# Optimization experiments

Measured on AMD Instinct MI355X. Metric: run time of the kernel, lower is better.

Reference implementation:

```python
import jax, jax.numpy as jnp
import numpy as np

DG = 8   # deformable groups
KK = 9   # 3x3 kernel positions


def conv3x3(x, w, b):
    # x: [B,C,H,W], w: [O,I,3,3] -> SAME conv, stride 1
    y = jax.lax.conv_general_dilated(x, w, (1, 1), 'SAME',
                                     dimension_numbers=('NCHW', 'OIHW', 'NCHW'))
    return y + b[None, :, None, None]


def modulated_deform_conv(x, offset, mask, w, b):
    # x: [B,C,H,W]; offset: [B,DG,KK,2,H,W] (dy,dx per group/kernel-pos);
    # mask: [B,DG,KK,H,W]; w: [O,C,3,3]; groups=1, stride=1, pad=1, dil=1.
    B, C, H, W = x.shape
    cg = C // DG  # channels per deformable group
    dy = offset[:, :, :, 0]  # [B,DG,KK,H,W]
    dx = offset[:, :, :, 1]
    ky, kx = jnp.meshgrid(jnp.arange(3), jnp.arange(3), indexing='ij')
    ky = (ky.reshape(KK) - 1).astype(x.dtype)  # kernel y offsets (pad=1)
    kx = (kx.reshape(KK) - 1).astype(x.dtype)
    py = dy + jnp.arange(H, dtype=x.dtype).reshape(1, 1, 1, H, 1) + ky.reshape(1, 1, KK, 1, 1)
    px = dx + jnp.arange(W, dtype=x.dtype).reshape(1, 1, 1, 1, W) + kx.reshape(1, 1, KK, 1, 1)
    y0 = jnp.floor(py)
    x0 = jnp.floor(px)
    ly = py - y0  # bilinear fractions
    lx = px - x0
    y0i = y0.astype(jnp.int32)
    x0i = x0.astype(jnp.int32)
    xf = x.reshape(B, DG, cg, H * W)

    def gather(yi, xi):
        # zero padding outside the image (per-corner validity)
        valid = ((yi >= 0) & (yi < H) & (xi >= 0) & (xi < W)).astype(x.dtype)
        idx = jnp.clip(yi, 0, H - 1) * W + jnp.clip(xi, 0, W - 1)  # [B,DG,KK,H,W]
        g = jnp.take_along_axis(xf, idx.reshape(B, DG, 1, KK * H * W), axis=-1)
        return g.reshape(B, DG, cg, KK, H, W) * valid[:, :, None]

    v = (((1 - ly) * (1 - lx))[:, :, None] * gather(y0i, x0i)
         + ((1 - ly) * lx)[:, :, None] * gather(y0i, x0i + 1)
         + (ly * (1 - lx))[:, :, None] * gather(y0i + 1, x0i)
         + (ly * lx)[:, :, None] * gather(y0i + 1, x0i + 1))
    v = (v * mask[:, :, None]).reshape(B, C, KK, H, W)  # modulated im2col
    out = jnp.einsum('bckhw,ock->bohw', v, w.reshape(w.shape[0], C, KK))
    return out + b[None, :, None, None]


def setup_inputs() -> dict:
    key = jax.random.key(0)
    ks = jax.random.split(key, 6)
    B, C, H, W = 8, 64, 128, 128
    f = lambda k, s: jax.random.normal(k, s, dtype=jnp.float32)
    return {
        'cat_fea': f(ks[0], (B, C, H, W)),
        'f_fea': f(ks[1], (B, C, H, W)),
        'w_off2d': f(ks[2], (C, C, 3, 3)) * 0.05,
        'b_off2d': jnp.zeros((C,), jnp.float32),
        'w_coff': f(ks[3], (3 * DG * KK, C, 3, 3)) * 0.01,  # small => near-zero offsets, as in DCNv2Pack init
        'b_coff': jnp.zeros((3 * DG * KK,), jnp.float32),
        'w_dconv': f(ks[4], (C, C, 3, 3)) * 0.05,
        'b_dconv': jnp.zeros((C,), jnp.float32),
    }


def reference(cat_fea, f_fea, w_off2d, b_off2d, w_coff, b_coff, w_dconv, b_dconv):
    # offset1 = self.off2d_1(cat_fea)
    offset_feat = conv3x3(cat_fea, w_off2d, b_off2d)
    # DCNv2Pack: conv_offset on the extra feature, chunk into o1,o2,mask
    off = conv3x3(offset_feat, w_coff, b_coff)  # [B, 3*DG*KK, H, W]
    o1, o2, m = jnp.split(off, 3, axis=1)
    B, _, H, W = off.shape
    # offset = cat(o1,o2); CUDA kernel reads channel ((g*KK+i)*2 + {0:y,1:x})
    offset = jnp.concatenate([o1, o2], axis=1).reshape(B, DG, KK, 2, H, W)
    mask = jax.nn.sigmoid(m).reshape(B, DG, KK, H, W)
    return modulated_deform_conv(f_fea, offset, mask, w_dconv, b_dconv)
```

## Files before the change

### kernel.cpp

```cpp
#include <hip/hip_runtime.h>
#include <math.h>

typedef __attribute__((ext_vector_type(4))) float f32x4;
typedef __attribute__((ext_vector_type(8))) short bf16x8;
typedef __attribute__((ext_vector_type(2))) _Float16 f16x2;
typedef __attribute__((ext_vector_type(8))) _Float16 f16x8;

#define HH 128
#define WW 128
#define HWSZ 16384
#define BHW 131072
#define BB 8

__device__ __forceinline__ float bf2f(ushort u) {
    union { uint i; float f; } x; x.i = ((uint)u) << 16; return x.f;
}
__device__ __forceinline__ ushort f2bf(float f) {
    union { float f; uint i; } x; x.f = f;
    uint r = (x.i + 0x7fffu + ((x.i >> 16) & 1u)) >> 16;
    return (ushort)r;
}
__device__ __forceinline__ ushort f2h_bits(float f) {
    union { _Float16 h; ushort u; } x; x.h = (_Float16)f; return x.u;
}

template<int F16>
__global__ __launch_bounds__(256) void to_gp_k(const float* __restrict__ x,
                                               ushort* __restrict__ y) {
    __shared__ ushort lds[64][66];
    int blk = blockIdx.x;
    int b = blk >> 8;
    int hw0 = (blk & 255) << 6;
    int t = threadIdx.x;
    int lane = t & 63;
    int q = t >> 6;
#pragma unroll
    for (int i = 0; i < 16; i++) {
        int c = i * 4 + q;
        float v = x[((size_t)(b * 64 + c) << 14) + hw0 + lane];
        lds[c][lane] = F16 ? f2h_bits(v) : f2bf(v);
    }
    __syncthreads();
#pragma unroll
    for (int it = 0; it < 2; it++) {
        int id = it * 256 + t;
        int cg = id >> 6;
        int px = id & 63;
        uint pk[4];
#pragma unroll
        for (int j = 0; j < 4; j++)
            pk[j] = (uint)lds[cg * 8 + 2 * j][px] | ((uint)lds[cg * 8 + 2 * j + 1][px] << 16);
        *(uint4*)(y + ((((size_t)b * 8 + cg) << 14) + hw0 + px) * 8) = *(uint4*)pk;
    }
}

template<int F16>
__global__ __launch_bounds__(256) void prep_wa(const float* __restrict__ w,
                                               ushort* __restrict__ wa, int Co, int Co_pad) {
    int idx = blockIdx.x * 256 + threadIdx.x;
    if (idx >= Co_pad * 576) return;
    int co = idx / 576, r = idx % 576;
    int kk = r >> 6, ci = r & 63;
    ushort v = 0;
    if (co < Co) {
        float f = w[(co * 64 + ci) * 9 + kk];
        v = F16 ? f2h_bits(f) : f2bf(f);
    }
    wa[idx] = v;
}

template<int COT, int MODE>
__global__ __launch_bounds__(256, 4) void conv_gemm3_k(
    const ushort* __restrict__ xt, const ushort* __restrict__ wa,
    const float* __restrict__ bias, ushort* __restrict__ y,
    uint* __restrict__ dyxp, ushort* __restrict__ mpl, int Cout) {
    constexpr int WCO = COT / 4;
    constexpr int NN = WCO / 16;
    constexpr int NA = COT / 32;
    __shared__ ushort Al[COT * 64];
    __shared__ ushort Bt[128 * 64];
    int t = threadIdx.x;
    int orig = blockIdx.x;
    int blk = (orig & 7) * 128 + (orig >> 3);
    int b = blk >> 7;
    int h = blk & 127;
    int cot = blockIdx.y;
    int lane = t & 63;
    int wv = t >> 6;
    int lg = lane >> 4;
    int lr = lane & 15;
    int rs = (lr & 7) << 4;
    int asw = ((lane & 7) ^ (lane >> 3)) << 4;
    const char* wab = (const char*)wa;

    f32x4 acc[NN][8];
#pragma unroll
    for (int n = 0; n < NN; n++)
#pragma unroll
        for (int j = 0; j < 8; j++) acc[n][j] = f32x4{0, 0, 0, 0};

#pragma unroll 1
    for (int kk = 0; kk < 9; kk++) {
        int ky = kk / 3;
        int kx = kk - ky * 3;
        __syncthreads();
#pragma unroll
        for (int a = 0; a < NA; a++) {
            int rb = wv * WCO + a * 8;
            const char* g = wab + (size_t)(cot * COT + rb + (lane >> 3)) * 1152 + kk * 128 + asw;
            __builtin_amdgcn_global_load_lds(
                (const __attribute__((address_space(1))) void*)g,
                (__attribute__((address_space(3))) void*)((char*)Al + rb * 128),
                16, 0, 0);
        }
        int hy = h + ky - 1;
        bool vr = (unsigned)hy < 128u;
#pragma unroll
        for (int i = 0; i < 4; i++) {
            int id = i * 256 + t;
            int px = id & 127;
            int cg = id >> 7;
            int wx = px + kx - 1;
            uint4 v = {0u, 0u, 0u, 0u};
            if (vr && (unsigned)wx < 128u)
                v = *(const uint4*)(xt + ((((size_t)b * 8 + cg) << 14) + (hy << 7) + wx) * 8);
            *(uint4*)((char*)Bt + px * 128 + ((cg * 16) ^ ((px & 7) << 4))) = v;
        }
        __syncthreads();
        bf16x8 a0[NN], a1[NN];
#pragma unroll
        for (int n = 0; n < NN; n++) {
            int ar = wv * WCO + n * 16 + lr;
            a0[n] = *(const bf16x8*)((char*)Al + ar * 128 + ((lg * 16) ^ rs));
            a1[n] = *(const bf16x8*)((char*)Al + ar * 128 + ((lg * 16 + 64) ^ rs));
        }
#pragma unroll
        for (int j = 0; j < 8; j++) {
            int pr = j * 16 + lr;
            bf16x8 b0 = *(const bf16x8*)((char*)Bt + pr * 128 + ((lg * 16) ^ rs));
            bf16x8 b1 = *(const bf16x8*)((char*)Bt + pr * 128 + ((lg * 16 + 64) ^ rs));
#pragma unroll
            for (int n = 0; n < NN; n++) {
                acc[n][j] = __builtin_amdgcn_mfma_f32_16x16x32_bf16(a0[n], b0, acc[n][j], 0, 0, 0);
                acc[n][j] = __builtin_amdgcn_mfma_f32_16x16x32_bf16(a1[n], b1, acc[n][j], 0, 0, 0);
            }
        }
    }

#pragma unroll
    for (int n = 0; n < NN; n++) {
        int co_g = cot * COT + wv * WCO + n * 16 + lg * 4;
        if (co_g < Cout) {
            float bs[4];
#pragma unroll
            for (int r = 0; r < 4; r++) bs[r] = bias[co_g + r];
#pragma unroll
            for (int j = 0; j < 8; j++) {
                int pxl = j * 16 + lr;
                int hw = (h << 7) + pxl;
                int bhw = (b << 14) + hw;
                if (MODE == 0) {
                    int cg = co_g >> 3, cs = co_g & 7;
                    uint2 s2;
                    s2.x = (uint)f2bf(acc[n][j][0] + bs[0]) | ((uint)f2bf(acc[n][j][1] + bs[1]) << 16);
                    s2.y = (uint)f2bf(acc[n][j][2] + bs[2]) | ((uint)f2bf(acc[n][j][3] + bs[3]) << 16);
                    *(uint2*)(y + ((((size_t)b * 8 + cg) << 14) + hw) * 8 + cs) = s2;
                } else if (co_g < 144) {
                    int p0 = co_g >> 1;
                    uint u0 = (uint)f2bf(acc[n][j][0] + bs[0]) | ((uint)f2bf(acc[n][j][1] + bs[1]) << 16);
                    uint u1 = (uint)f2bf(acc[n][j][2] + bs[2]) | ((uint)f2bf(acc[n][j][3] + bs[3]) << 16);
                    dyxp[(size_t)p0 * BHW + bhw] = u0;
                    dyxp[(size_t)(p0 + 1) * BHW + bhw] = u1;
                } else {
#pragma unroll
                    for (int r = 0; r < 4; r++) {
                        float f = 1.f / (1.f + __expf(-(acc[n][j][r] + bs[r])));
                        mpl[(size_t)(co_g - 144 + r) * BHW + bhw] = f2bf(f);
                    }
                }
            }
        }
    }
}

__global__ __launch_bounds__(256) void sample_k(
    const ushort* __restrict__ xg, const uint* __restrict__ dyxp,
    const ushort* __restrict__ mpl, ushort* __restrict__ vt) {
    int p = blockIdx.y;
    int dg = p / 9, tap = p - dg * 9;
    int ky = tap / 3, kx = tap - ky * 3;
    int bx = blockIdx.x;
    int bxs = (bx & 7) * 64 + (bx >> 3);
    int bhw = (bxs << 8) + threadIdx.x;
    int b = bhw >> 14;
    int h = (bhw >> 7) & 127;
    int w = bhw & 127;

    uint dyx = dyxp[(size_t)p * BHW + bhw];
    float m = bf2f(mpl[(size_t)p * BHW + bhw]);
    float dy = bf2f((ushort)(dyx & 0xffff));
    float dx = bf2f((ushort)(dyx >> 16));
    float py = dy + (float)(h + ky - 1);
    float px_ = dx + (float)(w + kx - 1);
    float fy = floorf(py), fx = floorf(px_);
    int y0 = (int)fy, x0 = (int)fx;
    int y1 = y0 + 1, x1 = x0 + 1;
    float ly = py - fy, lx = px_ - fx;
    bool vy0 = (unsigned)y0 < 128u, vy1 = (unsigned)y1 < 128u;
    bool vx0 = (unsigned)x0 < 128u, vx1 = (unsigned)x1 < 128u;
    float w00 = (vy0 && vx0) ? (1.f - ly) * (1.f - lx) * m : 0.f;
    float w01 = (vy0 && vx1) ? (1.f - ly) * lx * m : 0.f;
    float w10 = (vy1 && vx0) ? ly * (1.f - lx) * m : 0.f;
    float w11 = (vy1 && vx1) ? ly * lx * m : 0.f;
    int y0c = min(max(y0, 0), 127), y1c = min(max(y1, 0), 127);
    int x0c = min(max(x0, 0), 127), x1c = min(max(x1, 0), 127);
    const ushort* gb = xg + (((size_t)b * 8 + dg) << 17);
    uint4 q00 = *(const uint4*)(gb + ((y0c << 7) + x0c) * 8);
    uint4 q01 = *(const uint4*)(gb + ((y0c << 7) + x1c) * 8);
    uint4 q10 = *(const uint4*)(gb + ((y1c << 7) + x0c) * 8);
    uint4 q11 = *(const uint4*)(gb + ((y1c << 7) + x1c) * 8);
    const ushort* u00 = (const ushort*)&q00;
    const ushort* u01 = (const ushort*)&q01;
    const ushort* u10 = (const ushort*)&q10;
    const ushort* u11 = (const ushort*)&q11;
    uint pk[4];
#pragma unroll
    for (int c2 = 0; c2 < 4; c2++) {
        float v0 = w00 * bf2f(u00[2*c2])   + w01 * bf2f(u01[2*c2])
                 + w10 * bf2f(u10[2*c2])   + w11 * bf2f(u11[2*c2]);
        float v1 = w00 * bf2f(u00[2*c2+1]) + w01 * bf2f(u01[2*c2+1])
                 + w10 * bf2f(u10[2*c2+1]) + w11 * bf2f(u11[2*c2+1]);
        pk[c2] = (uint)f2bf(v0) | ((uint)f2bf(v1) << 16);
    }
    *(uint4*)(vt + ((size_t)p * BHW + bhw) * 8) = *(uint4*)pk;
}

__global__ __launch_bounds__(256, 3) void dgemm_k(
    const ushort* __restrict__ vt, const ushort* __restrict__ wa,
    const float* __restrict__ bias, float* __restrict__ out) {
    __shared__ ushort Al[64 * 64];
    __shared__ ushort Bt[64 * 64];
    int t = threadIdx.x;
    int orig = blockIdx.x;
    int blk = (orig & 7) * 256 + (orig >> 3);
    int b = blk >> 8;
    int h = (blk >> 1) & 127;
    int w0 = (blk & 1) << 6;
    int lane = t & 63;
    int wv = t >> 6;
    int lg = lane >> 4;
    int lr = lane & 15;
    int rs = (lr & 7) << 4;
    int asw = ((lane & 7) ^ (lane >> 3)) << 4;
    const char* wab = (const char*)wa;
    int bhw0 = (b << 14) + (h << 7) + w0;

    f32x4 acc[4] = {f32x4{0,0,0,0}, f32x4{0,0,0,0}, f32x4{0,0,0,0}, f32x4{0,0,0,0}};

#pragma unroll 1
    for (int kk = 0; kk < 9; kk++) {
        __syncthreads();
#pragma unroll
        for (int a = 0; a < 2; a++) {
            int rb = wv * 16 + a * 8;
            const char* g = wab + (size_t)(rb + (lane >> 3)) * 1152 + kk * 128 + asw;
            __builtin_amdgcn_global_load_lds(
                (const __attribute__((address_space(1))) void*)g,
                (__attribute__((address_space(3))) void*)((char*)Al + rb * 128),
                16, 0, 0);
        }
        uint4 v0 = *(const uint4*)(vt + ((size_t)(wv * 9 + kk) * BHW + bhw0 + lane) * 8);
        uint4 v1 = *(const uint4*)(vt + ((size_t)((wv + 4) * 9 + kk) * BHW + bhw0 + lane) * 8);
        int swl = (lane & 7) << 4;
        *(uint4*)((char*)Bt + lane * 128 + ((wv * 16) ^ swl)) = v0;
        *(uint4*)((char*)Bt + lane * 128 + (((wv + 4) * 16) ^ swl)) = v1;
        __syncthreads();
        int ar = wv * 16 + lr;
        bf16x8 a0 = *(const bf16x8*)((char*)Al + ar * 128 + ((lg * 16) ^ rs));
        bf16x8 a1 = *(const bf16x8*)((char*)Al + ar * 128 + ((lg * 16 + 64) ^ rs));
#pragma unroll
        for (int j = 0; j < 4; j++) {
            int pr = j * 16 + lr;
            bf16x8 b0 = *(const bf16x8*)((char*)Bt + pr * 128 + ((lg * 16) ^ rs));
            bf16x8 b1 = *(const bf16x8*)((char*)Bt + pr * 128 + ((lg * 16 + 64) ^ rs));
            acc[j] = __builtin_amdgcn_mfma_f32_16x16x32_bf16(a0, b0, acc[j], 0, 0, 0);
            acc[j] = __builtin_amdgcn_mfma_f32_16x16x32_bf16(a1, b1, acc[j], 0, 0, 0);
        }
    }

    int co_g = wv * 16 + lg * 4;
    float bs[4];
#pragma unroll
    for (int r = 0; r < 4; r++) bs[r] = bias[co_g + r];
#pragma unroll
    for (int j = 0; j < 4; j++) {
        int hw = (h << 7) + w0 + j * 16 + lr;
#pragma unroll
        for (int r = 0; r < 4; r++) {
            out[((size_t)(b * 64 + co_g + r) << 14) + hw] = acc[j][r] + bs[r];
        }
    }
}

__global__ __launch_bounds__(256, 3) void deform_reg3_k(
    const ushort* __restrict__ xg, const uint* __restrict__ dyxp,
    const ushort* __restrict__ mpl, const ushort* __restrict__ wa,
    const float* __restrict__ bias, float* __restrict__ out) {
    int t = threadIdx.x;
    int orig = blockIdx.x;
    int blk = (orig & 7) * 256 + (orig >> 3);
    int b = blk >> 8;
    int h = (blk >> 1) & 127;
    int w0 = (blk & 1) << 6;
    int lane = t & 63;
    int wv = t >> 6;
    int lg = lane >> 4;
    int lr = lane & 15;
    int wabs = w0 + wv * 16 + lr;
    int bhw = (b << 14) + (h << 7) + wabs;

    uint dyxv[18];
    float mv[18];
#pragma unroll
    for (int c = 0; c < 18; c++) {
        int dg = ((c & 1) << 2) + lg;
        int tap = c >> 1;
        dyxv[c] = dyxp[(size_t)(dg * 9 + tap) * BHW + bhw];
        mv[c] = bf2f(mpl[(size_t)(dg * 9 + tap) * BHW + bhw]);
    }

    uint4 qg[2][4];
    f32x4 wt4[2];
    f16x8 afr[2][4];
    f32x4 acc[4] = {f32x4{0,0,0,0}, f32x4{0,0,0,0}, f32x4{0,0,0,0}, f32x4{0,0,0,0}};

#define DPRE(c) do {                                                            \
    const int tap = (c) >> 1;                                                   \
    const int ky = tap / 3;                                                     \
    const int kx = tap - ky * 3;                                                \
    int dg = (((c) & 1) << 2) + lg;                                             \
    uint dyx = dyxv[(c)];                                                       \
    float dy = bf2f((ushort)(dyx & 0xffff));                                    \
    float dx = bf2f((ushort)(dyx >> 16));                                       \
    float py = dy + (float)(h + ky - 1);                                        \
    float px_ = dx + (float)(wabs + kx - 1);                                    \
    float fy = floorf(py), fx = floorf(px_);                                    \
    int y0 = (int)fy, x0 = (int)fx;                                             \
    int y1 = y0 + 1, x1 = x0 + 1;                                               \
    int y0c = min(max(y0, 0), 127), y1c = min(max(y1, 0), 127);                 \
    int x0c = min(max(x0, 0), 127), x1c = min(max(x1, 0), 127);                 \
    const ushort* gb = xg + (((size_t)b * 8 + dg) << 17);                       \
    qg[(c) & 1][0] = *(const uint4*)(gb + ((y0c << 7) + x0c) * 8);              \
    qg[(c) & 1][1] = *(const uint4*)(gb + ((y0c << 7) + x1c) * 8);              \
    qg[(c) & 1][2] = *(const uint4*)(gb + ((y1c << 7) + x0c) * 8);              \
    qg[(c) & 1][3] = *(const uint4*)(gb + ((y1c << 7) + x1c) * 8);              \
    float ly = py - fy, lx = px_ - fx;                                          \
    bool vy0 = (unsigned)y0 < 128u, vy1 = (unsigned)y1 < 128u;                  \
    bool vx0 = (unsigned)x0 < 128u, vx1 = (unsigned)x1 < 128u;                  \
    float m = mv[(c)];                                                          \
    f32x4 wv4;                                                                  \
    wv4[0] = (vy0 && vx0) ? (1.f - ly) * (1.f - lx) * m : 0.f;                  \
    wv4[1] = (vy0 && vx1) ? (1.f - ly) * lx * m : 0.f;                          \
    wv4[2] = (vy1 && vx0) ? ly * (1.f - lx) * m : 0.f;                          \
    wv4[3] = (vy1 && vx1) ? ly * lx * m : 0.f;                                  \
    wt4[(c) & 1] = wv4;                                                         \
} while (0)

#define APRE(c) do {                                                            \
    const ushort* wac = wa + (c) * 32 + lg * 8;                                 \
    _Pragma("unroll")                                                           \
    for (int n = 0; n < 4; n++)                                                 \
        afr[(c) & 1][n] = *(const f16x8*)(wac + (size_t)(n * 16 + lr) * 576);   \
} while (0)

    DPRE(0);
    APRE(0);

#pragma unroll
    for (int c = 0; c < 18; c++) {
        if (c < 17) {
            DPRE(c + 1);
            APRE(c + 1);
        }
        __builtin_amdgcn_sched_barrier(0);
        f32x4 wc = wt4[c & 1];
        _Float16 wh0 = (_Float16)wc[0], wh1 = (_Float16)wc[1];
        _Float16 wh2 = (_Float16)wc[2], wh3 = (_Float16)wc[3];
        f16x2 w0p = {wh0, wh0}, w1p = {wh1, wh1}, w2p = {wh2, wh2}, w3p = {wh3, wh3};
        union { uint4 u4; uint u[4]; } c00, c01, c10, c11;
        c00.u4 = qg[c & 1][0]; c01.u4 = qg[c & 1][1];
        c10.u4 = qg[c & 1][2]; c11.u4 = qg[c & 1][3];
        union { f16x2 p[4]; f16x8 v; } bf;
#pragma unroll
        for (int c2 = 0; c2 < 4; c2++) {
            union { uint u; f16x2 h; } h00, h01, h10, h11;
            h00.u = c00.u[c2]; h01.u = c01.u[c2];
            h10.u = c10.u[c2]; h11.u = c11.u[c2];
            bf.p[c2] = h00.h * w0p + h01.h * w1p + h10.h * w2p + h11.h * w3p;
        }
#pragma unroll
        for (int n = 0; n < 4; n++)
            acc[n] = __builtin_amdgcn_mfma_f32_16x16x32_f16(afr[c & 1][n], bf.v, acc[n], 0, 0, 0);
    }
#undef DPRE
#undef APRE

    int hw = (h << 7) + wabs;
#pragma unroll
    for (int n = 0; n < 4; n++) {
        int co_g = n * 16 + lg * 4;
#pragma unroll
        for (int r = 0; r < 4; r++) {
            out[((size_t)(b * 64 + co_g + r) << 14) + hw] = acc[n][r] + bias[co_g + r];
        }
    }
}

extern "C" void kernel_launch(void* const* d_in, const int* in_sizes, int n_in,
                              void* d_out, int out_size, void* d_ws, size_t ws_size,
                              hipStream_t stream) {
    const float* cat_fea = (const float*)d_in[0];
    const float* f_fea   = (const float*)d_in[1];
    const float* w_off2d = (const float*)d_in[2];
    const float* b_off2d = (const float*)d_in[3];
    const float* w_coff  = (const float*)d_in[4];
    const float* b_coff  = (const float*)d_in[5];
    const float* w_dconv = (const float*)d_in[6];
    const float* b_dconv = (const float*)d_in[7];
    float* out = (float*)d_out;

    const size_t NEED_SG = 224837632ull;

    if (ws_size >= NEED_SG) {
        ushort* xft  = (ushort*)d_ws;
        uint*   dyxp = (uint*)(xft + 8388608);
        ushort* mpl  = (ushort*)(dyxp + 9437184);
        ushort* wa1  = mpl + 9437184;
        ushort* wa2  = wa1 + 36864;
        ushort* wad  = wa2 + 147456;
        ushort* vt   = wad + 36864;
        ushort* x1t      = vt;
        ushort* off_feat = vt + 8388608;

        to_gp_k<0><<<2048, 256, 0, stream>>>(cat_fea, x1t);
        to_gp_k<0><<<2048, 256, 0, stream>>>(f_fea, xft);
        prep_wa<0><<<(64 * 576 + 255) / 256, 256, 0, stream>>>(w_off2d, wa1, 64, 64);
        prep_wa<0><<<(256 * 576 + 255) / 256, 256, 0, stream>>>(w_coff, wa2, 216, 256);
        prep_wa<0><<<(64 * 576 + 255) / 256, 256, 0, stream>>>(w_dconv, wad, 64, 64);

        conv_gemm3_k<64, 0><<<dim3(1024, 1), 256, 0, stream>>>(x1t, wa1, b_off2d, off_feat,
                                                               nullptr, nullptr, 64);
        conv_gemm3_k<128, 1><<<dim3(1024, 2), 256, 0, stream>>>(off_feat, wa2, b_coff, nullptr,
                                                                dyxp, mpl, 216);
        sample_k<<<dim3(512, 72), 256, 0, stream>>>(xft, dyxp, mpl, vt);
        dgemm_k<<<2048, 256, 0, stream>>>(vt, wad, b_dconv, out);
    } else {
        ushort* x1t      = (ushort*)d_ws;
        ushort* xft      = x1t + 8388608;
        ushort* off_feat = xft + 8388608;
        uint*   dyxp     = (uint*)(off_feat + 8388608);
        ushort* mpl      = (ushort*)(dyxp + 9437184);
        ushort* wa1      = mpl + 9437184;
        ushort* wa2      = wa1 + 36864;
        ushort* wad      = wa2 + 147456;

        to_gp_k<0><<<2048, 256, 0, stream>>>(cat_fea, x1t);
        to_gp_k<1><<<2048, 256, 0, stream>>>(f_fea, xft);
        prep_wa<0><<<(64 * 576 + 255) / 256, 256, 0, stream>>>(w_off2d, wa1, 64, 64);
        prep_wa<0><<<(256 * 576 + 255) / 256, 256, 0, stream>>>(w_coff, wa2, 216, 256);
        prep_wa<1><<<(64 * 576 + 255) / 256, 256, 0, stream>>>(w_dconv, wad, 64, 64);

        conv_gemm3_k<64, 0><<<dim3(1024, 1), 256, 0, stream>>>(x1t, wa1, b_off2d, off_feat,
                                                               nullptr, nullptr, 64);
        conv_gemm3_k<128, 1><<<dim3(1024, 2), 256, 0, stream>>>(off_feat, wa2, b_coff, nullptr,
                                                                dyxp, mpl, 216);
        deform_reg3_k<<<2048, 256, 0, stream>>>(xft, dyxp, mpl, wad, b_dconv, out);
    }
}
```

Baseline: 170.6 us.

## Use zero-padded inputs and double-buffered async LDS staging in conv GEMMs

The two regular 3x3 convolutions now read from a zero-padded 130x130 channel-grouped layout, so the input tile can be copied straight to LDS with global_load_lds and no bounds checks. The A and B tiles are double-buffered so the next kernel position's loads overlap the current MFMA work, and one barrier per iteration is removed. New small kernels zero the halo, and the first conv writes its output into a padded buffer for the second. The cost is twice the LDS per block (launch bound lowered to 2 blocks per CU), a different unswizzled LDS read pattern that may bank-conflict, and extra launches and workspace.

```diff
diff --git a/kernel.cpp b/kernel.cpp
--- a/kernel.cpp
+++ b/kernel.cpp
@@ -11,6 +11,7 @@
 #define HWSZ 16384
 #define BHW 131072
 #define BB 8
+#define PIMG (130 * 130 * 8)
 
 __device__ __forceinline__ float bf2f(ushort u) {
     union { uint i; float f; } x; x.i = ((uint)u) << 16; return x.f;
@@ -52,6 +53,49 @@
             pk[j] = (uint)lds[cg * 8 + 2 * j][px] | ((uint)lds[cg * 8 + 2 * j + 1][px] << 16);
         *(uint4*)(y + ((((size_t)b * 8 + cg) << 14) + hw0 + px) * 8) = *(uint4*)pk;
     }
+}
+
+__global__ __launch_bounds__(256) void to_gp_pad_k(const float* __restrict__ x,
+                                                   ushort* __restrict__ Pg) {
+    __shared__ ushort lds[64][66];
+    int blk = blockIdx.x;
+    int b = blk >> 8;
+    int hw0 = (blk & 255) << 6;
+    int t = threadIdx.x;
+    int lane = t & 63;
+    int q = t >> 6;
+#pragma unroll
+    for (int i = 0; i < 16; i++) {
+        int c = i * 4 + q;
+        lds[c][lane] = f2bf(x[((size_t)(b * 64 + c) << 14) + hw0 + lane]);
+    }
+    __syncthreads();
+#pragma unroll
+    for (int it = 0; it < 2; it++) {
+        int id = it * 256 + t;
+        int cg = id >> 6;
+        int px = id & 63;
+        uint pk[4];
+#pragma unroll
+        for (int j = 0; j < 4; j++)
+            pk[j] = (uint)lds[cg * 8 + 2 * j][px] | ((uint)lds[cg * 8 + 2 * j + 1][px] << 16);
+        int hw = hw0 + px;
+        int h = hw >> 7, w = hw & 127;
+        *(uint4*)(Pg + ((size_t)((b * 8 + cg) * 130 + h + 1) * 130 + w + 1) * 8) = *(uint4*)pk;
+    }
+}
+
+__global__ __launch_bounds__(256) void halo_zero_k(ushort* __restrict__ Pg) {
+    int idx = blockIdx.x * 256 + threadIdx.x;
+    if (idx >= 64 * 516) return;
+    int img = idx / 516, e = idx - img * 516;
+    int r, c;
+    if (e < 130)      { r = 0;           c = e; }
+    else if (e < 260) { r = 129;         c = e - 130; }
+    else if (e < 388) { r = e - 260 + 1; c = 0; }
+    else              { r = e - 388 + 1; c = 129; }
+    uint4 z = {0u, 0u, 0u, 0u};
+    *(uint4*)(Pg + ((size_t)(img * 130 + r) * 130 + c) * 8) = z;
 }
 
 template<int F16>
@@ -70,15 +114,16 @@
 }
 
 template<int COT, int MODE>
-__global__ __launch_bounds__(256, 4) void conv_gemm3_k(
-    const ushort* __restrict__ xt, const ushort* __restrict__ wa,
-    const float* __restrict__ bias, ushort* __restrict__ y,
+__global__ __launch_bounds__(256, 2) void conv_pad_k(
+    const ushort* __restrict__ Pg, const ushort* __restrict__ wa,
+    const float* __restrict__ bias, ushort* __restrict__ Pgo,
     uint* __restrict__ dyxp, ushort* __restrict__ mpl, int Cout) {
     constexpr int WCO = COT / 4;
     constexpr int NN = WCO / 16;
     constexpr int NA = COT / 32;
-    __shared__ ushort Al[COT * 64];
-    __shared__ ushort Bt[128 * 64];
+    constexpr int ABYTES = COT * 128;
+    __shared__ ushort Al[2 * COT * 64];
+    __shared__ ushort Bg[2 * 8192];
     int t = threadIdx.x;
     int orig = blockIdx.x;
     int blk = (orig & 7) * 128 + (orig >> 3);
@@ -93,59 +138,63 @@
     int asw = ((lane & 7) ^ (lane >> 3)) << 4;
     const char* wab = (const char*)wa;
 
+#define STAGE(KK, BI) do {                                                      \
+    int ky_ = (KK) / 3, kx_ = (KK) - ky_ * 3;                                   \
+    _Pragma("unroll")                                                           \
+    for (int a = 0; a < NA; a++) {                                              \
+        int rb = wv * WCO + a * 8;                                              \
+        const char* g = wab + (size_t)(cot * COT + rb + (lane >> 3)) * 1152 + (KK) * 128 + asw; \
+        __builtin_amdgcn_global_load_lds(                                       \
+            (const __attribute__((address_space(1))) void*)g,                   \
+            (__attribute__((address_space(3))) void*)((char*)Al + (BI) * ABYTES + rb * 128), \
+            16, 0, 0);                                                          \
+    }                                                                           \
+    _Pragma("unroll")                                                           \
+    for (int i = 0; i < 4; i++) {                                               \
+        int u = i * 4 + wv;                                                     \
+        int cg = u >> 1, hf = u & 1;                                            \
+        const char* g = (const char*)Pg +                                       \
+            ((size_t)((b * 8 + cg) * 130 + h + ky_) * 130 + kx_ + hf * 64 + lane) * 16; \
+        __builtin_amdgcn_global_load_lds(                                       \
+            (const __attribute__((address_space(1))) void*)g,                   \
+            (__attribute__((address_space(3))) void*)((char*)Bg + (BI) * 16384 + (cg * 128 + hf * 64) * 16), \
+            16, 0, 0);                                                          \
+    } } while (0)
+
     f32x4 acc[NN][8];
 #pragma unroll
     for (int n = 0; n < NN; n++)
 #pragma unroll
         for (int j = 0; j < 8; j++) acc[n][j] = f32x4{0, 0, 0, 0};
+
+    STAGE(0, 0);
+    __syncthreads();
 
 #pragma unroll 1
     for (int kk = 0; kk < 9; kk++) {
-        int ky = kk / 3;
-        int kx = kk - ky * 3;
-        __syncthreads();
-#pragma unroll
-        for (int a = 0; a < NA; a++) {
-            int rb = wv * WCO + a * 8;
-            const char* g = wab + (size_t)(cot * COT + rb + (lane >> 3)) * 1152 + kk * 128 + asw;
-            __builtin_amdgcn_global_load_lds(
-                (const __attribute__((address_space(1))) void*)g,
-                (__attribute__((address_space(3))) void*)((char*)Al + rb * 128),
-                16, 0, 0);
-        }
-        int hy = h + ky - 1;
-        bool vr = (unsigned)hy < 128u;
-#pragma unroll
-        for (int i = 0; i < 4; i++) {
-            int id = i * 256 + t;
-            int px = id & 127;
-            int cg = id >> 7;
-            int wx = px + kx - 1;
-            uint4 v = {0u, 0u, 0u, 0u};
-            if (vr && (unsigned)wx < 128u)
-                v = *(const uint4*)(xt + ((((size_t)b * 8 + cg) << 14) + (hy << 7) + wx) * 8);
-            *(uint4*)((char*)Bt + px * 128 + ((cg * 16) ^ ((px & 7) << 4))) = v;
-        }
-        __syncthreads();
+        int bi = kk & 1;
+        if (kk < 8) STAGE(kk + 1, bi ^ 1);
         bf16x8 a0[NN], a1[NN];
 #pragma unroll
         for (int n = 0; n < NN; n++) {
             int ar = wv * WCO + n * 16 + lr;
-            a0[n] = *(const bf16x8*)((char*)Al + ar * 128 + ((lg * 16) ^ rs));
-            a1[n] = *(const bf16x8*)((char*)Al + ar * 128 + ((lg * 16 + 64) ^ rs));
+            a0[n] = *(const bf16x8*)((char*)Al + bi * ABYTES + ar * 128 + ((lg * 16) ^ rs));
+            a1[n] = *(const bf16x8*)((char*)Al + bi * ABYTES + ar * 128 + ((lg * 16 + 64) ^ rs));
         }
 #pragma unroll
         for (int j = 0; j < 8; j++) {
             int pr = j * 16 + lr;
-            bf16x8 b0 = *(const bf16x8*)((char*)Bt + pr * 128 + ((lg * 16) ^ rs));
-            bf16x8 b1 = *(const bf16x8*)((char*)Bt + pr * 128 + ((lg * 16 + 64) ^ rs));
+            bf16x8 b0 = *(const bf16x8*)((char*)Bg + bi * 16384 + (lg * 128 + pr) * 16);
+            bf16x8 b1 = *(const bf16x8*)((char*)Bg + bi * 16384 + ((4 + lg) * 128 + pr) * 16);
 #pragma unroll
             for (int n = 0; n < NN; n++) {
                 acc[n][j] = __builtin_amdgcn_mfma_f32_16x16x32_bf16(a0[n], b0, acc[n][j], 0, 0, 0);
                 acc[n][j] = __builtin_amdgcn_mfma_f32_16x16x32_bf16(a1[n], b1, acc[n][j], 0, 0, 0);
             }
         }
-    }
+        __syncthreads();
+    }
+#undef STAGE
 
 #pragma unroll
     for (int n = 0; n < NN; n++) {
@@ -164,7 +213,7 @@
                     uint2 s2;
                     s2.x = (uint)f2bf(acc[n][j][0] + bs[0]) | ((uint)f2bf(acc[n][j][1] + bs[1]) << 16);
                     s2.y = (uint)f2bf(acc[n][j][2] + bs[2]) | ((uint)f2bf(acc[n][j][3] + bs[3]) << 16);
-                    *(uint2*)(y + ((((size_t)b * 8 + cg) << 14) + hw) * 8 + cs) = s2;
+                    *(uint2*)(Pgo + ((size_t)((b * 8 + cg) * 130 + h + 1) * 130 + pxl + 1) * 8 + cs) = s2;
                 } else if (co_g < 144) {
                     int p0 = co_g >> 1;
                     uint u0 = (uint)f2bf(acc[n][j][0] + bs[0]) | ((uint)f2bf(acc[n][j][1] + bs[1]) << 16);
@@ -439,41 +488,45 @@
         ushort* wa2  = wa1 + 36864;
         ushort* wad  = wa2 + 147456;
         ushort* vt   = wad + 36864;
-        ushort* x1t      = vt;
-        ushort* off_feat = vt + 8388608;
-
-        to_gp_k<0><<<2048, 256, 0, stream>>>(cat_fea, x1t);
+        ushort* Pg1  = vt;
+        ushort* Pgo  = vt + 8652800;
+
+        halo_zero_k<<<(64 * 516 + 255) / 256, 256, 0, stream>>>(Pg1);
+        halo_zero_k<<<(64 * 516 + 255) / 256, 256, 0, stream>>>(Pgo);
+        to_gp_pad_k<<<2048, 256, 0, stream>>>(cat_fea, Pg1);
         to_gp_k<0><<<2048, 256, 0, stream>>>(f_fea, xft);
         prep_wa<0><<<(64 * 576 + 255) / 256, 256, 0, stream>>>(w_off2d, wa1, 64, 64);
         prep_wa<0><<<(256 * 576 + 255) / 256, 256, 0, stream>>>(w_coff, wa2, 216, 256);
         prep_wa<0><<<(64 * 576 + 255) / 256, 256, 0, stream>>>(w_dconv, wad, 64, 64);
 
-        conv_gemm3_k<64, 0><<<dim3(1024, 1), 256, 0, stream>>>(x1t, wa1, b_off2d, off_feat,
-                                                               nullptr, nullptr, 64);
-        conv_gemm3_k<128, 1><<<dim3(1024, 2), 256, 0, stream>>>(off_feat, wa2, b_coff, nullptr,
-                                                                dyxp, mpl, 216);
+        conv_pad_k<64, 0><<<dim3(1024, 1), 256, 0, stream>>>(Pg1, wa1, b_off2d, Pgo,
+                                                             nullptr, nullptr, 64);
+        conv_pad_k<128, 1><<<dim3(1024, 2), 256, 0, stream>>>(Pgo, wa2, b_coff, nullptr,
+                                                              dyxp, mpl, 216);
         sample_k<<<dim3(512, 72), 256, 0, stream>>>(xft, dyxp, mpl, vt);
         dgemm_k<<<2048, 256, 0, stream>>>(vt, wad, b_dconv, out);
     } else {
-        ushort* x1t      = (ushort*)d_ws;
-        ushort* xft      = x1t + 8388608;
-        ushort* off_feat = xft + 8388608;
-        uint*   dyxp     = (uint*)(off_feat + 8388608);
-        ushort* mpl      = (ushort*)(dyxp + 9437184);
-        ushort* wa1      = mpl + 9437184;
-        ushort* wa2      = wa1 + 36864;
-        ushort* wad      = wa2 + 147456;
-
-        to_gp_k<0><<<2048, 256, 0, stream>>>(cat_fea, x1t);
+        ushort* Pg1  = (ushort*)d_ws;
+        ushort* Pgo  = Pg1 + 8652800;
+        ushort* xft  = Pgo + 8652800;
+        uint*   dyxp = (uint*)(xft + 8388608);
+        ushort* mpl  = (ushort*)(dyxp + 9437184);
+        ushort* wa1  = mpl + 9437184;
+        ushort* wa2  = wa1 + 36864;
+        ushort* wad  = wa2 + 147456;
+
+        halo_zero_k<<<(64 * 516 + 255) / 256, 256, 0, stream>>>(Pg1);
+        halo_zero_k<<<(64 * 516 + 255) / 256, 256, 0, stream>>>(Pgo);
+        to_gp_pad_k<<<2048, 256, 0, stream>>>(cat_fea, Pg1);
         to_gp_k<1><<<2048, 256, 0, stream>>>(f_fea, xft);
         prep_wa<0><<<(64 * 576 + 255) / 256, 256, 0, stream>>>(w_off2d, wa1, 64, 64);
         prep_wa<0><<<(256 * 576 + 255) / 256, 256, 0, stream>>>(w_coff, wa2, 216, 256);
         prep_wa<1><<<(64 * 576 + 255) / 256, 256, 0, stream>>>(w_dconv, wad, 64, 64);
 
-        conv_gemm3_k<64, 0><<<dim3(1024, 1), 256, 0, stream>>>(x1t, wa1, b_off2d, off_feat,
-                                                               nullptr, nullptr, 64);
-        conv_gemm3_k<128, 1><<<dim3(1024, 2), 256, 0, stream>>>(off_feat, wa2, b_coff, nullptr,
-                                                                dyxp, mpl, 216);
+        conv_pad_k<64, 0><<<dim3(1024, 1), 256, 0, stream>>>(Pg1, wa1, b_off2d, Pgo,
+                                                             nullptr, nullptr, 64);
+        conv_pad_k<128, 1><<<dim3(1024, 2), 256, 0, stream>>>(Pgo, wa2, b_coff, nullptr,
+                                                              dyxp, mpl, 216);
         deform_reg3_k<<<2048, 256, 0, stream>>>(xft, dyxp, mpl, wad, b_dconv, out);
     }
 }
```

Result: slower. 185.6 us (+8.8%).
